# Kernel optimization log

Hardware: AMD Instinct MI355X
Metric: run time of the kernel (lower is better)

The kernel has to match this reference:

```python
import jax, jax.numpy as jnp
import numpy as np

N_NODES = 100000
NUM_GRAPHS = 128
NEG_SLOPE = 0.2


def gat_layer(x, ei, W, a_src, a_dst, b, heads, ch, concat):
    """PyG-style GATConv (v1) with self-loops already included in ei.
    ei[0]=source j, ei[1]=target i; softmax over incoming edges of each target."""
    N = x.shape[0]
    h = (x @ W).reshape(N, heads, ch)                      # [N,H,C]
    asrc = jnp.sum(h * a_src, axis=-1)                     # [N,H]
    adst = jnp.sum(h * a_dst, axis=-1)                     # [N,H]
    src, dst = ei[0], ei[1]
    e = jax.nn.leaky_relu(asrc[src] + adst[dst], NEG_SLOPE)  # [E,H]
    m = jax.ops.segment_max(e, dst, num_segments=N)        # stable softmax per target
    ex = jnp.exp(e - m[dst])
    denom = jax.ops.segment_sum(ex, dst, num_segments=N)
    alpha = ex / denom[dst]                                # [E,H]
    msg = h[src] * alpha[:, :, None]                       # [E,H,C] gather+weight
    out = jax.ops.segment_sum(msg, dst, num_segments=N)    # scatter-add aggregate
    out = out.reshape(N, heads * ch) if concat else out.mean(axis=1)
    return out + b


def setup_inputs() -> dict:
    key = jax.random.key(0)
    ks = jax.random.split(key, 16)
    d_in = 128
    x = jax.random.normal(ks[0], (N_NODES, d_in), dtype=jnp.float32)
    edge_index = jax.random.randint(ks[1], (2, 1600000), 0, N_NODES, dtype=jnp.int64)
    batch = jnp.sort(jax.random.randint(ks[2], (N_NODES,), 0, NUM_GRAPHS, dtype=jnp.int64))
    s = lambda k, shp, fan: jax.random.normal(k, shp, dtype=jnp.float32) / np.sqrt(fan)
    params = dict(
        W1=s(ks[3], (d_in, 4 * 48), d_in),
        a_src1=0.1 * jax.random.normal(ks[4], (4, 48), dtype=jnp.float32),
        a_dst1=0.1 * jax.random.normal(ks[5], (4, 48), dtype=jnp.float32),
        b1=jnp.zeros((4 * 48,), dtype=jnp.float32),
        W2=s(ks[6], (192, 96), 192),
        a_src2=0.1 * jax.random.normal(ks[7], (1, 96), dtype=jnp.float32),
        a_dst2=0.1 * jax.random.normal(ks[8], (1, 96), dtype=jnp.float32),
        b2=jnp.zeros((96,), dtype=jnp.float32),
        fc1_w=s(ks[9], (96, 192), 96),
        fc1_b=jnp.zeros((192,), dtype=jnp.float32),
        fc2_w=s(ks[10], (192, 96), 192),
        fc2_b=jnp.zeros((96,), dtype=jnp.float32),
    )
    return dict(x=x, edge_index=edge_index, batch=batch, **params)


def reference(x, edge_index, batch, W1, a_src1, a_dst1, b1, W2, a_src2, a_dst2, b2,
              fc1_w, fc1_b, fc2_w, fc2_b):
    N = x.shape[0]
    loops = jnp.arange(N, dtype=edge_index.dtype)
    ei = jnp.concatenate([edge_index, jnp.stack([loops, loops])], axis=1)
    h = jax.nn.relu(gat_layer(x, ei, W1, a_src1, a_dst1, b1, heads=4, ch=48, concat=True))
    h = jax.nn.relu(gat_layer(h, ei, W2, a_src2, a_dst2, b2, heads=1, ch=96, concat=True))
    # global mean pool over graphs
    sums = jax.ops.segment_sum(h, batch, num_segments=NUM_GRAPHS)          # [G,96]
    counts = jax.ops.segment_sum(jnp.ones((N,), h.dtype), batch, num_segments=NUM_GRAPHS)
    pooled = sums / jnp.maximum(counts, 1.0)[:, None]
    z = jax.nn.relu(pooled @ fc1_w + fc1_b)
    return z @ fc2_w + fc2_b
```

## Files before the change

kernel.cpp:

```cpp
#include <hip/hip_runtime.h>


#define LRELU(x) fmaxf((x), 0.2f * (x))

using bf16x8 = __attribute__((ext_vector_type(8))) short;
using f32x16 = __attribute__((ext_vector_type(16))) float;

#define NSB 256

__device__ inline unsigned short f2bf(float f) {
  unsigned u = __builtin_bit_cast(unsigned, f);
  return (unsigned short)((u + 0x7fffu + ((u >> 16) & 1u)) >> 16);
}
__device__ inline float bf2f(unsigned short h) {
  return __builtin_bit_cast(float, (unsigned)h << 16);
}
__device__ inline float bfLO(unsigned v) { return __builtin_bit_cast(float, v << 16); }
__device__ inline float bfHI(unsigned v) { return __builtin_bit_cast(float, v & 0xffff0000u); }
__device__ inline unsigned packbf(float a, float b) {
  return (unsigned)f2bf(a) | ((unsigned)f2bf(b) << 16);
}

__device__ inline void wave_lds_fence() {
  __builtin_amdgcn_wave_barrier();
  __builtin_amdgcn_s_waitcnt(0xc07f);
  __builtin_amdgcn_wave_barrier();
}


__global__ __launch_bounds__(256) void k_hist2(const int* __restrict__ dst, int E, int chunk,
                                               int NBK, int* __restrict__ cntmat) {
  __shared__ int lh[512];
  int b = blockIdx.x, t = threadIdx.x;
  for (int i = t; i < NBK; i += 256) lh[i] = 0;
  __syncthreads();
  int beg = b * chunk, end = min(E, beg + chunk);
  for (int e = beg + t; e < end; e += 256) atomicAdd(&lh[dst[e] >> 8], 1);
  __syncthreads();
  for (int i = t; i < NBK; i += 256) cntmat[i * NSB + b] = lh[i];
}

__global__ __launch_bounds__(256) void k_rowscan(int* __restrict__ cntmat,
                                                 int* __restrict__ bucket_tot) {
  int k = blockIdx.x, t = threadIdx.x;
  __shared__ int sc[256];
  int v = cntmat[k * NSB + t];
  sc[t] = v;
  __syncthreads();
  for (int off = 1; off < 256; off <<= 1) {
    int add = (t >= off) ? sc[t - off] : 0;
    __syncthreads();
    sc[t] += add;
    __syncthreads();
  }
  cntmat[k * NSB + t] = sc[t] - v;
  if (t == 255) bucket_tot[k] = sc[t];
}

__global__ __launch_bounds__(512) void k_bscan(const int* __restrict__ bucket_tot, int NBK,
                                               int* __restrict__ bucket_off,
                                               int* __restrict__ row_off, int N, int E) {
  __shared__ int sc[512];
  int t = threadIdx.x;
  int v = (t < NBK) ? bucket_tot[t] : 0;
  sc[t] = v;
  __syncthreads();
  for (int off = 1; off < 512; off <<= 1) {
    int add = (t >= off) ? sc[t - off] : 0;
    __syncthreads();
    sc[t] += add;
    __syncthreads();
  }
  int excl = sc[t] - v;
  if (t < NBK) {
    bucket_off[t] = excl;
    if (t == NBK - 1) bucket_off[NBK] = excl + v;
  }
  if (t == 0) row_off[N] = E + N;
}

__global__ __launch_bounds__(256) void k_scatter2(const int* __restrict__ src,
                                                  const int* __restrict__ dst, int E, int chunk,
                                                  int NBK, const int* __restrict__ bucket_off,
                                                  const int* __restrict__ cntmat,
                                                  int* __restrict__ pairs) {
  __shared__ int base[512];
  __shared__ int cur[512];
  int b = blockIdx.x, t = threadIdx.x;
  for (int i = t; i < NBK; i += 256) {
    base[i] = bucket_off[i] + cntmat[i * NSB + b];
    cur[i] = 0;
  }
  __syncthreads();
  int beg = b * chunk, end = min(E, beg + chunk);
  for (int e = beg + t; e < end; e += 256) {
    int s = src[e], d = dst[e];
    int k = d >> 8;
    int loc = atomicAdd(&cur[k], 1);
    pairs[base[k] + loc] = (s << 8) | (d & 255);
  }
}

#define BBUILD_CAP 8448
__global__ __launch_bounds__(256) void k_bbuild(const int* __restrict__ pairs,
                                                const int* __restrict__ bucket_off,
                                                int N, int* __restrict__ row_off,
                                                int* __restrict__ col) {
  int b = blockIdx.x;
  int t = threadIdx.x;
  int base_d = b * 256;
  int nd = N - base_d;
  if (nd > 256) nd = 256;
  int pbeg = bucket_off[b], pend = bucket_off[b + 1];
  int cntb = pend - pbeg;
  int colbase = pbeg + base_d;

  __shared__ int hist[256];
  __shared__ int scn[256];
  __shared__ int cur[256];
  __shared__ int colL[BBUILD_CAP];
  hist[t] = 0;
  __syncthreads();
  for (int p = pbeg + t; p < pend; p += 256) atomicAdd(&hist[pairs[p] & 255], 1);
  __syncthreads();
  int v = (t < nd) ? hist[t] + 1 : 0;
  scn[t] = v;
  __syncthreads();
  for (int off = 1; off < 256; off <<= 1) {
    int add = (t >= off) ? scn[t - off] : 0;
    __syncthreads();
    scn[t] += add;
    __syncthreads();
  }
  int excl = scn[t] - v;
  if (t < nd) row_off[base_d + t] = colbase + excl;
  int total = cntb + nd;
  if (total <= BBUILD_CAP) {
    cur[t] = excl;
    if (t < nd) colL[excl + hist[t]] = base_d + t;
    __syncthreads();
    for (int p = pbeg + t; p < pend; p += 256) {
      int w = pairs[p];
      int lp = atomicAdd(&cur[w & 255], 1);
      colL[lp] = w >> 8;
    }
    __syncthreads();
    for (int i = t; i < total; i += 256) col[colbase + i] = colL[i];
  } else {
    cur[t] = excl;
    if (t < nd) col[colbase + excl + hist[t]] = base_d + t;
    __syncthreads();
    for (int p = pbeg + t; p < pend; p += 256) {
      int w = pairs[p];
      int lp = atomicAdd(&cur[w & 255], 1);
      col[colbase + lp] = w >> 8;
    }
  }
}


__global__ __launch_bounds__(256) void k_convW(const float* __restrict__ W, int K, int N,
                                               unsigned short* __restrict__ Th,
                                               unsigned short* __restrict__ Tl) {
  int idx = blockIdx.x * 256 + threadIdx.x;
  if (idx >= K * N) return;
  int k = idx / N, n = idx - k * N;
  float w = W[idx];
  unsigned short hi = f2bf(w);
  unsigned short lo = f2bf(w - bf2f(hi));
  Th[n * K + k] = hi;
  Tl[n * K + k] = lo;
}


template <int K, int N, bool A_BF16>
__global__ __launch_bounds__(256) void k_gemm_mfma(const void* __restrict__ Ap,
                                                   const unsigned short* __restrict__ Bh,
                                                   const unsigned short* __restrict__ Bl,
                                                   unsigned short* __restrict__ C, int M) {
  constexpr int NT = N / 32;
  __shared__ unsigned short As[128 * 40];
  __shared__ unsigned short Bhs[N * 40];
  __shared__ unsigned short Bls[N * 40];
  int tid = threadIdx.x;
  int wave = tid >> 6, lane = tid & 63;
  int bm = blockIdx.x * 128;

  f32x16 acc[NT];
#pragma unroll
  for (int t = 0; t < NT; ++t)
#pragma unroll
    for (int i = 0; i < 16; ++i) acc[t][i] = 0.f;

  for (int k0 = 0; k0 < K; k0 += 32) {
#pragma unroll
    for (int i = 0; i < 2; ++i) {
      int unit = tid + i * 256;
      int r = unit >> 2, u = unit & 3;
      int gr = bm + r;
      uint4 o = make_uint4(0, 0, 0, 0);
      if (gr < M) {
        if (A_BF16) {
          o = *(const uint4*)((const unsigned short*)Ap + (size_t)gr * K + k0 + u * 8);
        } else {
          const float* af = (const float*)Ap + (size_t)gr * K + k0 + u * 8;
          float4 v0 = *(const float4*)af;
          float4 v1 = *(const float4*)(af + 4);
          o.x = (unsigned)f2bf(v0.x) | ((unsigned)f2bf(v0.y) << 16);
          o.y = (unsigned)f2bf(v0.z) | ((unsigned)f2bf(v0.w) << 16);
          o.z = (unsigned)f2bf(v1.x) | ((unsigned)f2bf(v1.y) << 16);
          o.w = (unsigned)f2bf(v1.z) | ((unsigned)f2bf(v1.w) << 16);
        }
      }
      *(uint4*)&As[r * 40 + u * 8] = o;
    }
    for (int unit = tid; unit < N * 4; unit += 256) {
      int n = unit >> 2, u = unit & 3;
      *(uint4*)&Bhs[n * 40 + u * 8] = *(const uint4*)&Bh[n * K + k0 + u * 8];
      *(uint4*)&Bls[n * 40 + u * 8] = *(const uint4*)&Bl[n * K + k0 + u * 8];
    }
    __syncthreads();

    int arow = wave * 32 + (lane & 31);
    int fo = (lane >> 5) * 8;
#pragma unroll
    for (int s = 0; s < 2; ++s) {
      bf16x8 af = *(const bf16x8*)&As[arow * 40 + s * 16 + fo];
#pragma unroll
      for (int t = 0; t < NT; ++t) {
        bf16x8 bh = *(const bf16x8*)&Bhs[(t * 32 + (lane & 31)) * 40 + s * 16 + fo];
        bf16x8 bl = *(const bf16x8*)&Bls[(t * 32 + (lane & 31)) * 40 + s * 16 + fo];
        acc[t] = __builtin_amdgcn_mfma_f32_32x32x16_bf16(af, bh, acc[t], 0, 0, 0);
        acc[t] = __builtin_amdgcn_mfma_f32_32x32x16_bf16(af, bl, acc[t], 0, 0, 0);
      }
    }
    __syncthreads();
  }

#pragma unroll
  for (int t = 0; t < NT; ++t) {
    int col = t * 32 + (lane & 31);
#pragma unroll
    for (int r = 0; r < 16; ++r) {
      int row = wave * 32 + (r & 3) + 8 * (r >> 2) + 4 * (lane >> 5);
      int gr = bm + row;
      if (gr < M) C[(size_t)gr * N + col] = f2bf(acc[t][r]);
    }
  }
}


__global__ __launch_bounds__(256) void k_coef1(const unsigned short* __restrict__ h,
                                               const float* __restrict__ a_src,
                                               const float* __restrict__ a_dst,
                                               float* __restrict__ asrc,
                                               float* __restrict__ adst, int N) {
  int node = blockIdx.x;
  int w = threadIdx.x >> 6, lane = threadIdx.x & 63;
  float ps = 0.f, pd = 0.f;
  if (lane < 48) {
    int c = w * 48 + lane;
    float hv = bf2f(h[(size_t)node * 192 + c]);
    ps = hv * a_src[c];
    pd = hv * a_dst[c];
  }
#pragma unroll
  for (int off = 32; off > 0; off >>= 1) {
    ps += __shfl_down(ps, off);
    pd += __shfl_down(pd, off);
  }
  if (lane == 0) {
    asrc[node * 4 + w] = ps;
    adst[node * 4 + w] = pd;
  }
}

__global__ __launch_bounds__(128) void k_coef2(const unsigned short* __restrict__ h,
                                               const float* __restrict__ a_src,
                                               const float* __restrict__ a_dst,
                                               float* __restrict__ asrc,
                                               float* __restrict__ adst, int N) {
  int node = blockIdx.x;
  int w = threadIdx.x >> 6, lane = threadIdx.x & 63;
  int c = w * 64 + lane;
  float ps = 0.f, pd = 0.f;
  if (c < 96) {
    float hv = bf2f(h[(size_t)node * 96 + c]);
    ps = hv * a_src[c];
    pd = hv * a_dst[c];
  }
#pragma unroll
  for (int off = 32; off > 0; off >>= 1) {
    ps += __shfl_down(ps, off);
    pd += __shfl_down(pd, off);
  }
  __shared__ float sp[2], sd[2];
  if (lane == 0) { sp[w] = ps; sd[w] = pd; }
  __syncthreads();
  if (threadIdx.x == 0) {
    asrc[node] = sp[0] + sp[1];
    adst[node] = sd[0] + sd[1];
  }
}


__global__ __launch_bounds__(256) void k_agg1(const unsigned short* __restrict__ h,
                                              const float* __restrict__ asrc,
                                              const float* __restrict__ adst,
                                              const int* __restrict__ row_off,
                                              const int* __restrict__ col,
                                              const float* __restrict__ b1,
                                              unsigned short* __restrict__ out, int N) {
  __shared__ int sL[4][64];
  __shared__ float wL[4][64][4];
  int wid = threadIdx.x >> 6;
  int node = blockIdx.x * 4 + wid;
  if (node >= N) return;
  int lane = threadIdx.x & 63;
  int half = lane >> 5;
  int m = lane & 31;
  int hA = m / 12;
  int hB = (m < 8) ? 2 : 3;
  int beg = __builtin_amdgcn_readfirstlane(row_off[node]);
  int end = __builtin_amdgcn_readfirstlane(row_off[node + 1]);
  float4 ad = *(const float4*)&adst[node * 4];
  float accA0 = 0, accA1 = 0, accA2 = 0, accA3 = 0, accB0 = 0, accB1 = 0;
  float da = 0.f, db = 0.f;
  const unsigned* h32 = (const unsigned*)h;
  for (int base = beg; base < end; base += 64) {
    int cnt = end - base;
    if (cnt > 64) cnt = 64;
    int s = 0;
    float w0 = 0.f, w1 = 0.f, w2 = 0.f, w3 = 0.f;
    if (lane < cnt) {
      s = col[base + lane];
      float4 as = *(const float4*)&asrc[s * 4];
      w0 = __expf(LRELU(as.x + ad.x));
      w1 = __expf(LRELU(as.y + ad.y));
      w2 = __expf(LRELU(as.z + ad.z));
      w3 = __expf(LRELU(as.w + ad.w));
    }
    sL[wid][lane] = s;
    *(float4*)&wL[wid][lane][0] = make_float4(w0, w1, w2, w3);
    wave_lds_fence();
    int jmax = (cnt + 1) & ~1;
#pragma unroll 2
    for (int j = 0; j < jmax; j += 2) {
      int je = j + half;
      int sj = sL[wid][je];
      float wa = wL[wid][je][hA];
      float wb = wL[wid][je][hB];
      const unsigned* hp = h32 + (size_t)sj * 96;
      uint2 va = *(const uint2*)(hp + 2 * m);
      unsigned vb = hp[64 + m];
      da += wa;
      db += wb;
      accA0 += wa * bfLO(va.x);
      accA1 += wa * bfHI(va.x);
      accA2 += wa * bfLO(va.y);
      accA3 += wa * bfHI(va.y);
      accB0 += wb * bfLO(vb);
      accB1 += wb * bfHI(vb);
    }
    __builtin_amdgcn_wave_barrier();
  }
  da += __shfl_xor(da, 32);
  db += __shfl_xor(db, 32);
  accA0 += __shfl_xor(accA0, 32);
  accA1 += __shfl_xor(accA1, 32);
  accA2 += __shfl_xor(accA2, 32);
  accA3 += __shfl_xor(accA3, 32);
  accB0 += __shfl_xor(accB0, 32);
  accB1 += __shfl_xor(accB1, 32);
  if (half == 0) {
    float ra = 1.f / da, rb = 1.f / db;
    float4 biA = *(const float4*)&b1[4 * m];
    float2 biB = *(const float2*)&b1[128 + 2 * m];
    unsigned* op = (unsigned*)(out + (size_t)node * 192);
    uint2 pa;
    pa.x = packbf(fmaxf(accA0 * ra + biA.x, 0.f), fmaxf(accA1 * ra + biA.y, 0.f));
    pa.y = packbf(fmaxf(accA2 * ra + biA.z, 0.f), fmaxf(accA3 * ra + biA.w, 0.f));
    *(uint2*)(op + 2 * m) = pa;
    op[64 + m] = packbf(fmaxf(accB0 * rb + biB.x, 0.f), fmaxf(accB1 * rb + biB.y, 0.f));
  }
}

__global__ __launch_bounds__(256) void k_agg2(const unsigned short* __restrict__ h,
                                              const float* __restrict__ asrc,
                                              const float* __restrict__ adst,
                                              const int* __restrict__ row_off,
                                              const int* __restrict__ col,
                                              const float* __restrict__ b2,
                                              float* __restrict__ out, int N) {
  __shared__ int2 eL[4][64];
  int wid = threadIdx.x >> 6;
  int node = blockIdx.x * 4 + wid;
  if (node >= N) return;
  int lane = threadIdx.x & 63;
  int half = lane >> 5;
  int m = lane & 31;
  int beg = __builtin_amdgcn_readfirstlane(row_off[node]);
  int end = __builtin_amdgcn_readfirstlane(row_off[node + 1]);
  float ad = adst[node];
  float acc0 = 0, acc1 = 0, acc2 = 0, acc3 = 0;
  float den = 0.f;
  const unsigned* h32 = (const unsigned*)h;
  for (int base = beg; base < end; base += 64) {
    int cnt = end - base;
    if (cnt > 64) cnt = 64;
    int s = 0;
    float w = 0.f;
    if (lane < cnt) {
      s = col[base + lane];
      w = __expf(LRELU(asrc[s] + ad));
    }
    eL[wid][lane] = make_int2(s, __builtin_bit_cast(int, w));
    wave_lds_fence();
    int jmax = (cnt + 1) & ~1;
#pragma unroll 2
    for (int j = 0; j < jmax; j += 2) {
      int2 e = eL[wid][j + half];
      int sj = e.x;
      float wj = __builtin_bit_cast(float, e.y);
      den += wj;
      if (m < 24) {
        uint2 v = *(const uint2*)(h32 + (size_t)sj * 48 + 2 * m);
        acc0 += wj * bfLO(v.x);
        acc1 += wj * bfHI(v.x);
        acc2 += wj * bfLO(v.y);
        acc3 += wj * bfHI(v.y);
      }
    }
    __builtin_amdgcn_wave_barrier();
  }
  den += __shfl_xor(den, 32);
  acc0 += __shfl_xor(acc0, 32);
  acc1 += __shfl_xor(acc1, 32);
  acc2 += __shfl_xor(acc2, 32);
  acc3 += __shfl_xor(acc3, 32);
  if (half == 0 && m < 24) {
    float r = 1.f / den;
    float4 bi = *(const float4*)&b2[4 * m];
    float4 o;
    o.x = fmaxf(acc0 * r + bi.x, 0.f);
    o.y = fmaxf(acc1 * r + bi.y, 0.f);
    o.z = fmaxf(acc2 * r + bi.z, 0.f);
    o.w = fmaxf(acc3 * r + bi.w, 0.f);
    *(float4*)&out[(size_t)node * 96 + 4 * m] = o;
  }
}


__global__ __launch_bounds__(384) void k_pool_mlp(const float* __restrict__ o2,
                                                  const int* __restrict__ batch, int N,
                                                  const float* __restrict__ fc1w,
                                                  const float* __restrict__ fc1b,
                                                  const float* __restrict__ fc2w,
                                                  const float* __restrict__ fc2b,
                                                  float* __restrict__ out) {
  int g = blockIdx.x;
  int t = threadIdx.x;
  int lo = 0, hi = N;
  while (lo < hi) { int mid = (lo + hi) >> 1; if (batch[mid] < g) lo = mid + 1; else hi = mid; }
  int lo2 = lo;
  int l = lo, hh = N;
  while (l < hh) { int mid = (l + hh) >> 1; if (batch[mid] < g + 1) l = mid + 1; else hh = mid; }
  int hi2 = l;

  __shared__ float part[4][96];
  __shared__ float pooled[96];
  __shared__ float z[192];
  int grp = t / 96, c = t % 96;
  float s = 0.f;
  for (int n = lo2 + grp; n < hi2; n += 4) s += o2[(size_t)n * 96 + c];
  part[grp][c] = s;
  __syncthreads();
  if (t < 96) {
    float tot = part[0][t] + part[1][t] + part[2][t] + part[3][t];
    pooled[t] = tot / fmaxf((float)(hi2 - lo2), 1.0f);
  }
  __syncthreads();
  if (t < 192) {
    float a = fc1b[t];
#pragma unroll 4
    for (int cc = 0; cc < 96; ++cc) a += pooled[cc] * fc1w[cc * 192 + t];
    z[t] = fmaxf(a, 0.f);
  }
  __syncthreads();
  if (t < 96) {
    float a = fc2b[t];
#pragma unroll 4
    for (int j = 0; j < 192; ++j) a += z[j] * fc2w[j * 96 + t];
    out[g * 96 + t] = a;
  }
}


extern "C" void kernel_launch(void* const* d_in, const int* in_sizes, int n_in,
                              void* d_out, int out_size, void* d_ws, size_t ws_size,
                              hipStream_t stream) {
  const float* x = (const float*)d_in[0];
  const int* ei = (const int*)d_in[1];
  const int* batch = (const int*)d_in[2];
  const float* W1 = (const float*)d_in[3];
  const float* a_src1 = (const float*)d_in[4];
  const float* a_dst1 = (const float*)d_in[5];
  const float* b1 = (const float*)d_in[6];
  const float* W2 = (const float*)d_in[7];
  const float* a_src2 = (const float*)d_in[8];
  const float* a_dst2 = (const float*)d_in[9];
  const float* b2 = (const float*)d_in[10];
  const float* fc1w = (const float*)d_in[11];
  const float* fc1b = (const float*)d_in[12];
  const float* fc2w = (const float*)d_in[13];
  const float* fc2b = (const float*)d_in[14];
  float* out = (float*)d_out;

  const int N = in_sizes[2];
  const int E = in_sizes[1] / 2;
  const int G = out_size / 96;
  const int NBK = (N + 255) >> 8;
  const int chunk = (E + NSB - 1) / NSB;

  size_t off = 0;
  auto alloc = [&](size_t bytes) {
    void* p = (char*)d_ws + off;
    off += (bytes + 255) & ~(size_t)255;
    return p;
  };
  unsigned short* h_bf = (unsigned short*)alloc((size_t)N * 192 * 2);
  unsigned short* o1_bf = (unsigned short*)alloc((size_t)N * 192 * 2);
  float* o2_f = (float*)alloc((size_t)N * 96 * 4);
  float* asrc1 = (float*)alloc((size_t)N * 4 * 4);
  float* adst1 = (float*)alloc((size_t)N * 4 * 4);
  float* asrc2 = (float*)alloc((size_t)N * 4);
  float* adst2 = (float*)alloc((size_t)N * 4);
  unsigned short* W1h = (unsigned short*)alloc((size_t)192 * 128 * 2);
  unsigned short* W1l = (unsigned short*)alloc((size_t)192 * 128 * 2);
  unsigned short* W2h = (unsigned short*)alloc((size_t)96 * 192 * 2);
  unsigned short* W2l = (unsigned short*)alloc((size_t)96 * 192 * 2);
  int* row_off = (int*)alloc((size_t)(N + 1) * 4);
  int* col = (int*)alloc((size_t)(E + N) * 4);
  int* pairs = (int*)alloc((size_t)E * 4);
  int* cntmat = (int*)alloc((size_t)NBK * NSB * 4);
  int* bucket_tot = (int*)alloc((size_t)NBK * 4);
  int* bucket_off = (int*)alloc((size_t)(NBK + 1) * 4);
  (void)ws_size;

  const int* src = ei;
  const int* dst = ei + E;

  k_convW<<<(128 * 192 + 255) / 256, 256, 0, stream>>>(W1, 128, 192, W1h, W1l);
  k_convW<<<(192 * 96 + 255) / 256, 256, 0, stream>>>(W2, 192, 96, W2h, W2l);

  k_hist2<<<NSB, 256, 0, stream>>>(dst, E, chunk, NBK, cntmat);
  k_rowscan<<<NBK, 256, 0, stream>>>(cntmat, bucket_tot);
  k_bscan<<<1, 512, 0, stream>>>(bucket_tot, NBK, bucket_off, row_off, N, E);
  k_scatter2<<<NSB, 256, 0, stream>>>(src, dst, E, chunk, NBK, bucket_off, cntmat, pairs);
  k_bbuild<<<NBK, 256, 0, stream>>>(pairs, bucket_off, N, row_off, col);

  int gblk = (N + 127) / 128;

  k_gemm_mfma<128, 192, false><<<gblk, 256, 0, stream>>>(x, W1h, W1l, h_bf, N);
  k_coef1<<<N, 256, 0, stream>>>(h_bf, a_src1, a_dst1, asrc1, adst1, N);
  k_agg1<<<(N + 3) / 4, 256, 0, stream>>>(h_bf, asrc1, adst1, row_off, col, b1, o1_bf, N);

  k_gemm_mfma<192, 96, true><<<gblk, 256, 0, stream>>>(o1_bf, W2h, W2l, h_bf, N);
  k_coef2<<<N, 128, 0, stream>>>(h_bf, a_src2, a_dst2, asrc2, adst2, N);
  k_agg2<<<(N + 3) / 4, 256, 0, stream>>>(h_bf, asrc2, adst2, row_off, col, b2, o2_f, N);

  k_pool_mlp<<<G, 384, 0, stream>>>(o2_f, batch, N, fc1w, fc1b, fc2w, fc2b, out);
}
```

Measured before the change: 552.7 us.

## Process more edges per wave in aggregation and pack coefficient kernels per wave

After: 517.4 us. 1.07x faster.

```diff
diff --git a/kernel.cpp b/kernel.cpp
--- a/kernel.cpp
+++ b/kernel.cpp
@@ -255,51 +255,78 @@
                                                const float* __restrict__ a_dst,
                                                float* __restrict__ asrc,
                                                float* __restrict__ adst, int N) {
-  int node = blockIdx.x;
-  int w = threadIdx.x >> 6, lane = threadIdx.x & 63;
-  float ps = 0.f, pd = 0.f;
-  if (lane < 48) {
-    int c = w * 48 + lane;
-    float hv = bf2f(h[(size_t)node * 192 + c]);
-    ps = hv * a_src[c];
-    pd = hv * a_dst[c];
-  }
-#pragma unroll
-  for (int off = 32; off > 0; off >>= 1) {
-    ps += __shfl_down(ps, off);
-    pd += __shfl_down(pd, off);
-  }
-  if (lane == 0) {
-    asrc[node * 4 + w] = ps;
-    adst[node * 4 + w] = pd;
-  }
-}
-
-__global__ __launch_bounds__(128) void k_coef2(const unsigned short* __restrict__ h,
+  int node = blockIdx.x * 4 + (threadIdx.x >> 6);
+  if (node >= N) return;
+  int m = threadIdx.x & 63;
+  const unsigned* hp = (const unsigned*)h + (size_t)node * 96;
+  unsigned va = hp[m];
+  float x0 = bfLO(va), x1 = bfHI(va);
+  float2 as = *(const float2*)&a_src[2 * m];
+  float2 ad = *(const float2*)&a_dst[2 * m];
+  float pas = x0 * as.x + x1 * as.y;
+  float pad = x0 * ad.x + x1 * ad.y;
+  int ha = m / 24;
+  float pbs = 0.f, pbd = 0.f;
+  int hb = (m < 8) ? 2 : 3;
+  if (m < 32) {
+    unsigned vb = hp[64 + m];
+    float y0 = bfLO(vb), y1 = bfHI(vb);
+    float2 bs = *(const float2*)&a_src[128 + 2 * m];
+    float2 bd = *(const float2*)&a_dst[128 + 2 * m];
+    pbs = y0 * bs.x + y1 * bs.y;
+    pbd = y0 * bd.x + y1 * bd.y;
+  }
+  float4 cs, cd;
+  cs.x = (ha == 0) ? pas : 0.f;
+  cs.y = (ha == 1) ? pas : 0.f;
+  cs.z = ((ha == 2) ? pas : 0.f) + ((hb == 2) ? pbs : 0.f);
+  cs.w = (hb == 3) ? pbs : 0.f;
+  cd.x = (ha == 0) ? pad : 0.f;
+  cd.y = (ha == 1) ? pad : 0.f;
+  cd.z = ((ha == 2) ? pad : 0.f) + ((hb == 2) ? pbd : 0.f);
+  cd.w = (hb == 3) ? pbd : 0.f;
+#pragma unroll
+  for (int off = 1; off < 64; off <<= 1) {
+    cs.x += __shfl_xor(cs.x, off);
+    cs.y += __shfl_xor(cs.y, off);
+    cs.z += __shfl_xor(cs.z, off);
+    cs.w += __shfl_xor(cs.w, off);
+    cd.x += __shfl_xor(cd.x, off);
+    cd.y += __shfl_xor(cd.y, off);
+    cd.z += __shfl_xor(cd.z, off);
+    cd.w += __shfl_xor(cd.w, off);
+  }
+  if (m == 0) {
+    *(float4*)&asrc[node * 4] = cs;
+    *(float4*)&adst[node * 4] = cd;
+  }
+}
+
+__global__ __launch_bounds__(256) void k_coef2(const unsigned short* __restrict__ h,
                                                const float* __restrict__ a_src,
                                                const float* __restrict__ a_dst,
                                                float* __restrict__ asrc,
                                                float* __restrict__ adst, int N) {
-  int node = blockIdx.x;
-  int w = threadIdx.x >> 6, lane = threadIdx.x & 63;
-  int c = w * 64 + lane;
+  int node = blockIdx.x * 4 + (threadIdx.x >> 6);
+  if (node >= N) return;
+  int m = threadIdx.x & 63;
   float ps = 0.f, pd = 0.f;
-  if (c < 96) {
-    float hv = bf2f(h[(size_t)node * 96 + c]);
-    ps = hv * a_src[c];
-    pd = hv * a_dst[c];
-  }
-#pragma unroll
-  for (int off = 32; off > 0; off >>= 1) {
-    ps += __shfl_down(ps, off);
-    pd += __shfl_down(pd, off);
-  }
-  __shared__ float sp[2], sd[2];
-  if (lane == 0) { sp[w] = ps; sd[w] = pd; }
-  __syncthreads();
-  if (threadIdx.x == 0) {
-    asrc[node] = sp[0] + sp[1];
-    adst[node] = sd[0] + sd[1];
+  if (m < 48) {
+    unsigned v = ((const unsigned*)h)[(size_t)node * 48 + m];
+    float x0 = bfLO(v), x1 = bfHI(v);
+    float2 as = *(const float2*)&a_src[2 * m];
+    float2 ad = *(const float2*)&a_dst[2 * m];
+    ps = x0 * as.x + x1 * as.y;
+    pd = x0 * ad.x + x1 * ad.y;
+  }
+#pragma unroll
+  for (int off = 1; off < 64; off <<= 1) {
+    ps += __shfl_xor(ps, off);
+    pd += __shfl_xor(pd, off);
+  }
+  if (m == 0) {
+    asrc[node] = ps;
+    adst[node] = pd;
   }
 }
 
@@ -317,14 +344,16 @@
   int node = blockIdx.x * 4 + wid;
   if (node >= N) return;
   int lane = threadIdx.x & 63;
-  int half = lane >> 5;
-  int m = lane & 31;
-  int hA = m / 12;
-  int hB = (m < 8) ? 2 : 3;
+  int q = lane >> 4;
+  int m = lane & 15;
+  int hA = m / 6;
+  int hB = (m < 4) ? 2 : 3;
   int beg = __builtin_amdgcn_readfirstlane(row_off[node]);
   int end = __builtin_amdgcn_readfirstlane(row_off[node + 1]);
   float4 ad = *(const float4*)&adst[node * 4];
-  float accA0 = 0, accA1 = 0, accA2 = 0, accA3 = 0, accB0 = 0, accB1 = 0;
+  float accA0 = 0, accA1 = 0, accA2 = 0, accA3 = 0;
+  float accA4 = 0, accA5 = 0, accA6 = 0, accA7 = 0;
+  float accB0 = 0, accB1 = 0, accB2 = 0, accB3 = 0;
   float da = 0.f, db = 0.f;
   const unsigned* h32 = (const unsigned*)h;
   for (int base = beg; base < end; base += 64) {
@@ -343,45 +372,55 @@
     sL[wid][lane] = s;
     *(float4*)&wL[wid][lane][0] = make_float4(w0, w1, w2, w3);
     wave_lds_fence();
-    int jmax = (cnt + 1) & ~1;
+    int jmax = (cnt + 3) & ~3;
 #pragma unroll 2
-    for (int j = 0; j < jmax; j += 2) {
-      int je = j + half;
+    for (int j = 0; j < jmax; j += 4) {
+      int je = j + q;
       int sj = sL[wid][je];
       float wa = wL[wid][je][hA];
       float wb = wL[wid][je][hB];
       const unsigned* hp = h32 + (size_t)sj * 96;
-      uint2 va = *(const uint2*)(hp + 2 * m);
-      unsigned vb = hp[64 + m];
+      uint4 va = *(const uint4*)(hp + 4 * m);
+      uint2 vb = *(const uint2*)(hp + 64 + 2 * m);
       da += wa;
       db += wb;
       accA0 += wa * bfLO(va.x);
       accA1 += wa * bfHI(va.x);
       accA2 += wa * bfLO(va.y);
       accA3 += wa * bfHI(va.y);
-      accB0 += wb * bfLO(vb);
-      accB1 += wb * bfHI(vb);
+      accA4 += wa * bfLO(va.z);
+      accA5 += wa * bfHI(va.z);
+      accA6 += wa * bfLO(va.w);
+      accA7 += wa * bfHI(va.w);
+      accB0 += wb * bfLO(vb.x);
+      accB1 += wb * bfHI(vb.x);
+      accB2 += wb * bfLO(vb.y);
+      accB3 += wb * bfHI(vb.y);
     }
     __builtin_amdgcn_wave_barrier();
   }
-  da += __shfl_xor(da, 32);
-  db += __shfl_xor(db, 32);
-  accA0 += __shfl_xor(accA0, 32);
-  accA1 += __shfl_xor(accA1, 32);
-  accA2 += __shfl_xor(accA2, 32);
-  accA3 += __shfl_xor(accA3, 32);
-  accB0 += __shfl_xor(accB0, 32);
-  accB1 += __shfl_xor(accB1, 32);
-  if (half == 0) {
+#define RED2(x) x += __shfl_xor(x, 16); x += __shfl_xor(x, 32)
+  RED2(da); RED2(db);
+  RED2(accA0); RED2(accA1); RED2(accA2); RED2(accA3);
+  RED2(accA4); RED2(accA5); RED2(accA6); RED2(accA7);
+  RED2(accB0); RED2(accB1); RED2(accB2); RED2(accB3);
+#undef RED2
+  if (q == 0) {
     float ra = 1.f / da, rb = 1.f / db;
-    float4 biA = *(const float4*)&b1[4 * m];
-    float2 biB = *(const float2*)&b1[128 + 2 * m];
+    float4 biA0 = *(const float4*)&b1[8 * m];
+    float4 biA1 = *(const float4*)&b1[8 * m + 4];
+    float4 biB = *(const float4*)&b1[128 + 4 * m];
     unsigned* op = (unsigned*)(out + (size_t)node * 192);
-    uint2 pa;
-    pa.x = packbf(fmaxf(accA0 * ra + biA.x, 0.f), fmaxf(accA1 * ra + biA.y, 0.f));
-    pa.y = packbf(fmaxf(accA2 * ra + biA.z, 0.f), fmaxf(accA3 * ra + biA.w, 0.f));
-    *(uint2*)(op + 2 * m) = pa;
-    op[64 + m] = packbf(fmaxf(accB0 * rb + biB.x, 0.f), fmaxf(accB1 * rb + biB.y, 0.f));
+    uint4 pa;
+    pa.x = packbf(fmaxf(accA0 * ra + biA0.x, 0.f), fmaxf(accA1 * ra + biA0.y, 0.f));
+    pa.y = packbf(fmaxf(accA2 * ra + biA0.z, 0.f), fmaxf(accA3 * ra + biA0.w, 0.f));
+    pa.z = packbf(fmaxf(accA4 * ra + biA1.x, 0.f), fmaxf(accA5 * ra + biA1.y, 0.f));
+    pa.w = packbf(fmaxf(accA6 * ra + biA1.z, 0.f), fmaxf(accA7 * ra + biA1.w, 0.f));
+    *(uint4*)(op + 4 * m) = pa;
+    uint2 pb;
+    pb.x = packbf(fmaxf(accB0 * rb + biB.x, 0.f), fmaxf(accB1 * rb + biB.y, 0.f));
+    pb.y = packbf(fmaxf(accB2 * rb + biB.z, 0.f), fmaxf(accB3 * rb + biB.w, 0.f));
+    *(uint2*)(op + 64 + 2 * m) = pb;
   }
 }
 
@@ -397,12 +436,13 @@
   int node = blockIdx.x * 4 + wid;
   if (node >= N) return;
   int lane = threadIdx.x & 63;
-  int half = lane >> 5;
-  int m = lane & 31;
+  int g = lane >> 3;
+  int m3 = lane & 7;
   int beg = __builtin_amdgcn_readfirstlane(row_off[node]);
   int end = __builtin_amdgcn_readfirstlane(row_off[node + 1]);
   float ad = adst[node];
-  float acc0 = 0, acc1 = 0, acc2 = 0, acc3 = 0;
+  float a0 = 0, a1 = 0, a2 = 0, a3 = 0, a4 = 0, a5 = 0;
+  float a6 = 0, a7 = 0, a8 = 0, a9 = 0, a10 = 0, a11 = 0;
   float den = 0.f;
   const unsigned* h32 = (const unsigned*)h;
   for (int base = beg; base < end; base += 64) {
@@ -416,37 +456,58 @@
     }
     eL[wid][lane] = make_int2(s, __builtin_bit_cast(int, w));
     wave_lds_fence();
-    int jmax = (cnt + 1) & ~1;
+    int jmax = (cnt + 7) & ~7;
 #pragma unroll 2
-    for (int j = 0; j < jmax; j += 2) {
-      int2 e = eL[wid][j + half];
+    for (int j = 0; j < jmax; j += 8) {
+      int2 e = eL[wid][j + g];
       int sj = e.x;
       float wj = __builtin_bit_cast(float, e.y);
       den += wj;
-      if (m < 24) {
-        uint2 v = *(const uint2*)(h32 + (size_t)sj * 48 + 2 * m);
-        acc0 += wj * bfLO(v.x);
-        acc1 += wj * bfHI(v.x);
-        acc2 += wj * bfLO(v.y);
-        acc3 += wj * bfHI(v.y);
-      }
+      const unsigned* hp = h32 + (size_t)sj * 48;
+      uint4 v0 = *(const uint4*)(hp + 4 * m3);
+      uint2 v1 = *(const uint2*)(hp + 32 + 2 * m3);
+      a0 += wj * bfLO(v0.x);
+      a1 += wj * bfHI(v0.x);
+      a2 += wj * bfLO(v0.y);
+      a3 += wj * bfHI(v0.y);
+      a4 += wj * bfLO(v0.z);
+      a5 += wj * bfHI(v0.z);
+      a6 += wj * bfLO(v0.w);
+      a7 += wj * bfHI(v0.w);
+      a8 += wj * bfLO(v1.x);
+      a9 += wj * bfHI(v1.x);
+      a10 += wj * bfLO(v1.y);
+      a11 += wj * bfHI(v1.y);
     }
     __builtin_amdgcn_wave_barrier();
   }
-  den += __shfl_xor(den, 32);
-  acc0 += __shfl_xor(acc0, 32);
-  acc1 += __shfl_xor(acc1, 32);
-  acc2 += __shfl_xor(acc2, 32);
-  acc3 += __shfl_xor(acc3, 32);
-  if (half == 0 && m < 24) {
+#define RED3(x) x += __shfl_xor(x, 8); x += __shfl_xor(x, 16); x += __shfl_xor(x, 32)
+  RED3(den);
+  RED3(a0); RED3(a1); RED3(a2); RED3(a3); RED3(a4); RED3(a5);
+  RED3(a6); RED3(a7); RED3(a8); RED3(a9); RED3(a10); RED3(a11);
+#undef RED3
+  if (lane < 8) {
     float r = 1.f / den;
-    float4 bi = *(const float4*)&b2[4 * m];
-    float4 o;
-    o.x = fmaxf(acc0 * r + bi.x, 0.f);
-    o.y = fmaxf(acc1 * r + bi.y, 0.f);
-    o.z = fmaxf(acc2 * r + bi.z, 0.f);
-    o.w = fmaxf(acc3 * r + bi.w, 0.f);
-    *(float4*)&out[(size_t)node * 96 + 4 * m] = o;
+    float* op = out + (size_t)node * 96;
+    float4 bi0 = *(const float4*)&b2[8 * m3];
+    float4 bi1 = *(const float4*)&b2[8 * m3 + 4];
+    float4 bi2 = *(const float4*)&b2[64 + 4 * m3];
+    float4 o0, o1, o2;
+    o0.x = fmaxf(a0 * r + bi0.x, 0.f);
+    o0.y = fmaxf(a1 * r + bi0.y, 0.f);
+    o0.z = fmaxf(a2 * r + bi0.z, 0.f);
+    o0.w = fmaxf(a3 * r + bi0.w, 0.f);
+    o1.x = fmaxf(a4 * r + bi1.x, 0.f);
+    o1.y = fmaxf(a5 * r + bi1.y, 0.f);
+    o1.z = fmaxf(a6 * r + bi1.z, 0.f);
+    o1.w = fmaxf(a7 * r + bi1.w, 0.f);
+    o2.x = fmaxf(a8 * r + bi2.x, 0.f);
+    o2.y = fmaxf(a9 * r + bi2.y, 0.f);
+    o2.z = fmaxf(a10 * r + bi2.z, 0.f);
+    o2.w = fmaxf(a11 * r + bi2.w, 0.f);
+    *(float4*)(op + 8 * m3) = o0;
+    *(float4*)(op + 8 * m3 + 4) = o1;
+    *(float4*)(op + 64 + 4 * m3) = o2;
   }
 }
 
@@ -560,14 +621,15 @@
   k_bbuild<<<NBK, 256, 0, stream>>>(pairs, bucket_off, N, row_off, col);
 
   int gblk = (N + 127) / 128;
+  int nblk4 = (N + 3) / 4;
 
   k_gemm_mfma<128, 192, false><<<gblk, 256, 0, stream>>>(x, W1h, W1l, h_bf, N);
-  k_coef1<<<N, 256, 0, stream>>>(h_bf, a_src1, a_dst1, asrc1, adst1, N);
-  k_agg1<<<(N + 3) / 4, 256, 0, stream>>>(h_bf, asrc1, adst1, row_off, col, b1, o1_bf, N);
+  k_coef1<<<nblk4, 256, 0, stream>>>(h_bf, a_src1, a_dst1, asrc1, adst1, N);
+  k_agg1<<<nblk4, 256, 0, stream>>>(h_bf, asrc1, adst1, row_off, col, b1, o1_bf, N);
 
   k_gemm_mfma<192, 96, true><<<gblk, 256, 0, stream>>>(o1_bf, W2h, W2l, h_bf, N);
-  k_coef2<<<N, 128, 0, stream>>>(h_bf, a_src2, a_dst2, asrc2, adst2, N);
-  k_agg2<<<(N + 3) / 4, 256, 0, stream>>>(h_bf, asrc2, adst2, row_off, col, b2, o2_f, N);
+  k_coef2<<<nblk4, 256, 0, stream>>>(h_bf, a_src2, a_dst2, asrc2, adst2, N);
+  k_agg2<<<nblk4, 256, 0, stream>>>(h_bf, asrc2, adst2, row_off, col, b2, o2_f, N);
 
   k_pool_mlp<<<G, 384, 0, stream>>>(o2_f, batch, N, fc1w, fc1b, fc2w, fc2b, out);
 }
```
